# Kernel tuning notes

Hardware: AMD Instinct MI355X
Metric: run time of the kernel (lower is better)

Reference implementation:

```python
import jax, jax.numpy as jnp
import numpy as np

HEAD = 4

def setup_inputs() -> dict:
    key = jax.random.key(0)
    ks = jax.random.split(key, 6)
    b, h, w, dim, attn_dim = 2, 64, 64, 256, 128
    return {
        "query": jax.random.normal(ks[0], (b, h, w, dim), jnp.float32),
        "context": jax.random.normal(ks[1], (b, h, w, dim), jnp.float32),
        "Wq": jax.random.normal(ks[2], (dim, attn_dim), jnp.float32) * (dim ** -0.5),
        "Wk": jax.random.normal(ks[3], (dim, attn_dim), jnp.float32) * (dim ** -0.5),
        "Wv": jax.random.normal(ks[4], (dim, attn_dim), jnp.float32) * (dim ** -0.5),
        "Wo": jax.random.normal(ks[5], (attn_dim, dim), jnp.float32) * (attn_dim ** -0.5),
    }

def reference(query, context, Wq, Wk, Wv, Wo):
    b, h, w, c = query.shape
    attn_dim = Wq.shape[1]
    head = HEAD
    head_dim = attn_dim // head
    scale = head_dim ** -0.5
    n = h * w
    # 1x1 conv, no bias == per-pixel dense projection
    q = (query.reshape(b, n, c) @ Wq).reshape(b, n, head, head_dim)
    k = (context.reshape(b, n, c) @ Wk).reshape(b, n, head, head_dim)
    v = (context.reshape(b, n, c) @ Wv).reshape(b, n, head, head_dim)
    score = jnp.einsum('bihd,bjhd->bijh', q, k) * scale  # [b, n, n, head]
    attn = jax.nn.softmax(score, axis=-2)  # softmax over key axis j
    out = jnp.einsum('bijh,bjhd->bihd', attn, v).reshape(b, n, attn_dim)
    return (out @ Wo).reshape(b, h, w, c)
```

## Files before the change

kernel.cpp:

```cpp
#include <hip/hip_runtime.h>
#include <hip/hip_bf16.h>
#include <math.h>

#define N_TOK 4096
#define C_DIM 256
#define A_DIM 128
#define HEADS 4
#define HD    32
#define NBAT  2
#define BH    (NBAT * HEADS)

#define SCALE_LOG2E 0.25503521f

#define SPLITS 8
#define KEYS_PER_SPLIT (N_TOK / SPLITS)

#define KS 40
#define VS 72
#define PS 40

typedef __attribute__((ext_vector_type(8))) short short8;
typedef __attribute__((ext_vector_type(4))) short short4_t;
typedef __attribute__((ext_vector_type(4))) float floatx4;

__device__ __forceinline__ unsigned short f2bf(float f) {
    unsigned int u = __float_as_uint(f);
    u = (u + 0x7fffu + ((u >> 16) & 1u)) >> 16;
    return (unsigned short)u;
}
__device__ __forceinline__ float bf2f(unsigned short u) {
    return __uint_as_float((unsigned int)u << 16);
}
__device__ __forceinline__ unsigned int pack2(float a, float b) {
    unsigned int lo = (__float_as_uint(a) + 0x8000u) >> 16;
    unsigned int hi = (__float_as_uint(b) + 0x8000u) & 0xffff0000u;
    return hi | lo;
}

__global__ __launch_bounds__(256) void wpack_kernel(
    const float* __restrict__ Wq, const float* __restrict__ Wk,
    const float* __restrict__ Wv, const float* __restrict__ Wo,
    unsigned short* __restrict__ Wp)
{
    const int chunk = blockIdx.x * 256 + threadIdx.x;
    const int wid = chunk >> 12;
    const int c = chunk & 4095;
    const int lane = c & 63, quad = lane >> 4, l15 = lane & 15;
    short8 v;
    if (wid < 3) {
        const int s = c >> 9, t = (c >> 6) & 7;
        const float* W = (wid == 0) ? Wq : ((wid == 1) ? Wk : Wv);
        const float scale = (wid == 0) ? SCALE_LOG2E : 1.0f;
        const int src = (s * 32 + quad * 8) * A_DIM + t * 16 + l15;
        #pragma unroll
        for (int j = 0; j < 8; j++) v[j] = (short)f2bf(W[src + j * A_DIM] * scale);
    } else {
        const int s = c >> 10, t = (c >> 6) & 15;
        const int src = (s * 32 + quad * 8) * C_DIM + t * 16 + l15;
        #pragma unroll
        for (int j = 0; j < 8; j++) v[j] = (short)f2bf(Wo[src + j * C_DIM]);
    }
    *(short8*)(Wp + (long)chunk * 8) = v;
}

__global__ __launch_bounds__(256) void qkv_kernel(
    const float* __restrict__ query, const float* __restrict__ context,
    const unsigned short* __restrict__ Wp,
    unsigned short* __restrict__ Qb, unsigned short* __restrict__ Kb,
    unsigned short* __restrict__ Vb)
{
    __shared__ __align__(16) unsigned short V_lds[128 * 18];

    const int tid = threadIdx.x;
    const int w = tid >> 6, lane = tid & 63;
    const int quad = lane >> 4, l15 = lane & 15;
    const int ch = w;
    const long i0 = (long)blockIdx.x * 16;
    const long row = i0 + l15;

    const unsigned short* Wqp = Wp;
    const unsigned short* Wkp = Wp + 32768;
    const unsigned short* Wvp = Wp + 65536;

    floatx4 aQ[2] = {}, aK[2] = {}, aV[2] = {};

    for (int s = 0; s < 8; s++) {
        const float* qp = query + row * C_DIM + s * 32 + quad * 8;
        const float* cp = context + row * C_DIM + s * 32 + quad * 8;
        floatx4 q0 = *(const floatx4*)qp, q1 = *(const floatx4*)(qp + 4);
        floatx4 c0 = *(const floatx4*)cp, c1 = *(const floatx4*)(cp + 4);
        short8 aq, ac;
        #pragma unroll
        for (int j = 0; j < 4; j++) {
            aq[j] = (short)f2bf(q0[j]); aq[4 + j] = (short)f2bf(q1[j]);
            ac[j] = (short)f2bf(c0[j]); ac[4 + j] = (short)f2bf(c1[j]);
        }
        #pragma unroll
        for (int tp = 0; tp < 2; tp++) {
            const long fo = ((long)(s * 8 + ch * 2 + tp) * 64 + lane) * 8;
            short8 bq = *(const short8*)(Wqp + fo);
            short8 bk = *(const short8*)(Wkp + fo);
            short8 bv = *(const short8*)(Wvp + fo);
            aQ[tp] = __builtin_amdgcn_mfma_f32_16x16x32_bf16(aq, bq, aQ[tp], 0, 0, 0);
            aK[tp] = __builtin_amdgcn_mfma_f32_16x16x32_bf16(ac, bk, aK[tp], 0, 0, 0);
            aV[tp] = __builtin_amdgcn_mfma_f32_16x16x32_bf16(ac, bv, aV[tp], 0, 0, 0);
        }
    }

    const long b = i0 >> 12;
    const long n0 = i0 & (N_TOK - 1);
    const long nbase = n0 + quad * 4;
    #pragma unroll
    for (int tp = 0; tp < 2; tp++) {
        const int col = ch * 32 + tp * 16 + l15;
        const int h = col >> 5, d = col & 31;
        unsigned short* qdst = Qb + ((b * HEADS + h) * N_TOK + nbase) * HD + d;
        unsigned short* kdst = Kb + ((b * HEADS + h) * N_TOK + nbase) * HD + d;
        #pragma unroll
        for (int r = 0; r < 4; r++) {
            qdst[r * HD] = f2bf(aQ[tp][r]);
            kdst[r * HD] = f2bf(aK[tp][r]);
        }
        short4_t pv;
        #pragma unroll
        for (int r = 0; r < 4; r++) pv[r] = (short)f2bf(aV[tp][r]);
        *(short4_t*)&V_lds[col * 18 + quad * 4] = pv;
    }
    __syncthreads();

    {
        const int col = tid >> 1, seg = tid & 1;
        const int h = col >> 5, d = col & 31;
        unsigned short* dst = Vb + ((b * HEADS + h) * HD + d) * N_TOK + n0 + seg * 8;
        *(short8*)dst = *(const short8*)&V_lds[col * 18 + seg * 8];
    }
}

__global__ __launch_bounds__(256, 4) void attn_kernel(
    const unsigned short* __restrict__ Qb, const unsigned short* __restrict__ Kb,
    const unsigned short* __restrict__ Vb,
    unsigned short* __restrict__ AO, float* __restrict__ Lbuf)
{
    __shared__ __align__(16) unsigned short K_lds[64 * KS];
    __shared__ __align__(16) unsigned short V_lds[HD * VS];
    __shared__ __align__(16) unsigned short P_lds[4][2][2 * 16 * PS];

    const int tid  = threadIdx.x;
    const int w    = tid >> 6;
    const int lane = tid & 63;
    const int quad = lane >> 4;
    const int l15  = lane & 15;

    const int L  = blockIdx.x;
    const int g  = (L & 7) + 8 * ((L >> 3) >> 5);
    const int qb = (L >> 3) & 31;
    const int bh = g & 7;
    const int z  = g >> 3;
    const int i0 = qb * 128 + w * 32;

    const unsigned short* Qh = Qb + (long)bh * N_TOK * HD;
    const unsigned short* Kh = Kb + (long)bh * N_TOK * HD;
    const unsigned short* Vh = Vb + (long)bh * HD * N_TOK;

    const short8 qfA = *(const short8*)(Qh + (long)(i0 + l15) * HD + quad * 8);
    const short8 qfB = *(const short8*)(Qh + (long)(i0 + 16 + l15) * HD + quad * 8);

    floatx4 accA0 = {0.f,0.f,0.f,0.f}, accA1 = {0.f,0.f,0.f,0.f};
    floatx4 accB0 = {0.f,0.f,0.f,0.f}, accB1 = {0.f,0.f,0.f,0.f};
    float lAc = 0.f, lBc = 0.f;

    const int  kst = (tid >> 2) * KS + (tid & 3) * 8;
    const int  vst = (tid >> 3) * VS + (tid & 7) * 8;
    const long vgl = (long)(tid >> 3) * N_TOK + (tid & 7) * 8;
    const int  pwb = l15 * (PS / 2);

    const int j_lo = z * KEYS_PER_SPLIT, j_hi = j_lo + KEYS_PER_SPLIT;

    short8 kreg = *(const short8*)(Kh + (long)j_lo * HD + tid * 8);
    short8 vreg = *(const short8*)(Vh + vgl + j_lo);

    for (int j0 = j_lo; j0 < j_hi; j0 += 64) {
        __syncthreads();
        *(short8*)&K_lds[kst] = kreg;
        *(short8*)&V_lds[vst] = vreg;
        if (j0 + 64 < j_hi) {
            kreg = *(const short8*)(Kh + (long)(j0 + 64) * HD + tid * 8);
            vreg = *(const short8*)(Vh + vgl + j0 + 64);
        }
        __syncthreads();

        #pragma unroll
        for (int sub = 0; sub < 2; sub++) {
            const int jb = sub * 32;
            short8 kf0 = *(short8*)&K_lds[(jb + l15) * KS + quad * 8];
            short8 kf1 = *(short8*)&K_lds[(jb + 16 + l15) * KS + quad * 8];
            const floatx4 zf = {0.f,0.f,0.f,0.f};
            floatx4 sA0 = __builtin_amdgcn_mfma_f32_16x16x32_bf16(kf0, qfA, zf, 0, 0, 0);
            floatx4 sA1 = __builtin_amdgcn_mfma_f32_16x16x32_bf16(kf1, qfA, zf, 0, 0, 0);
            floatx4 sB0 = __builtin_amdgcn_mfma_f32_16x16x32_bf16(kf0, qfB, zf, 0, 0, 0);
            floatx4 sB1 = __builtin_amdgcn_mfma_f32_16x16x32_bf16(kf1, qfB, zf, 0, 0, 0);

            floatx4 pA0, pA1, pB0, pB1;
            #pragma unroll
            for (int r = 0; r < 4; r++) {
                pA0[r] = __builtin_amdgcn_exp2f(sA0[r]);
                pA1[r] = __builtin_amdgcn_exp2f(sA1[r]);
                pB0[r] = __builtin_amdgcn_exp2f(sB0[r]);
                pB1[r] = __builtin_amdgcn_exp2f(sB1[r]);
                lAc += pA0[r] + pA1[r];
                lBc += pB0[r] + pB1[r];
            }

            unsigned int* Pq = (unsigned int*)&P_lds[w][sub][0];
            Pq[pwb + quad * 2 + 0]       = pack2(pA0[0], pA0[1]);
            Pq[pwb + quad * 2 + 1]       = pack2(pA0[2], pA0[3]);
            Pq[pwb + 8 + quad * 2 + 0]   = pack2(pA1[0], pA1[1]);
            Pq[pwb + 8 + quad * 2 + 1]   = pack2(pA1[2], pA1[3]);
            Pq[320 + pwb + quad * 2 + 0] = pack2(pB0[0], pB0[1]);
            Pq[320 + pwb + quad * 2 + 1] = pack2(pB0[2], pB0[3]);
            Pq[320 + pwb + 8 + quad * 2 + 0] = pack2(pB1[0], pB1[1]);
            Pq[320 + pwb + 8 + quad * 2 + 1] = pack2(pB1[2], pB1[3]);

            short8 pfA = *(short8*)&P_lds[w][sub][l15 * PS + quad * 8];
            short8 pfB = *(short8*)&P_lds[w][sub][16 * PS + l15 * PS + quad * 8];

            short8 vf0 = *(short8*)&V_lds[l15 * VS + jb + quad * 8];
            short8 vf1 = *(short8*)&V_lds[(16 + l15) * VS + jb + quad * 8];
            accA0 = __builtin_amdgcn_mfma_f32_16x16x32_bf16(pfA, vf0, accA0, 0, 0, 0);
            accA1 = __builtin_amdgcn_mfma_f32_16x16x32_bf16(pfA, vf1, accA1, 0, 0, 0);
            accB0 = __builtin_amdgcn_mfma_f32_16x16x32_bf16(pfB, vf0, accB0, 0, 0, 0);
            accB1 = __builtin_amdgcn_mfma_f32_16x16x32_bf16(pfB, vf1, accB1, 0, 0, 0);
        }
    }

    lAc += __shfl_xor(lAc, 16); lAc += __shfl_xor(lAc, 32);
    lBc += __shfl_xor(lBc, 16); lBc += __shfl_xor(lBc, 32);

    const int b = bh >> 2, h = bh & 3;
    unsigned short* AOz = AO + (long)z * (NBAT * N_TOK * A_DIM);
    float* Lz = Lbuf + (long)z * (BH * N_TOK);
    if (quad == 0) {
        Lz[(long)bh * N_TOK + i0 + l15]      = lAc;
        Lz[(long)bh * N_TOK + i0 + 16 + l15] = lBc;
    }
    #pragma unroll
    for (int r = 0; r < 4; r++) {
        const float invA = 1.0f / __shfl(lAc, quad * 4 + r);
        const float invB = 1.0f / __shfl(lBc, quad * 4 + r);
        const long rowA = (long)b * N_TOK + i0 + quad * 4 + r;
        const long rowB = rowA + 16;
        AOz[rowA * A_DIM + h * HD + l15]      = f2bf(accA0[r] * invA);
        AOz[rowA * A_DIM + h * HD + 16 + l15] = f2bf(accA1[r] * invA);
        AOz[rowB * A_DIM + h * HD + l15]      = f2bf(accB0[r] * invB);
        AOz[rowB * A_DIM + h * HD + 16 + l15] = f2bf(accB1[r] * invB);
    }
}

__global__ __launch_bounds__(256) void outproj_kernel(
    const unsigned short* __restrict__ AO, const float* __restrict__ Lbuf,
    const unsigned short* __restrict__ Wp, float* __restrict__ out)
{
    const int tid = threadIdx.x;
    const int w = tid >> 6, lane = tid & 63;
    const int quad = lane >> 4, l15 = lane & 15;
    const int ch = w;
    const long i0 = (long)blockIdx.x * 16;
    const long row = i0 + l15;
    const int b = (int)(row >> 12);
    const int n = (int)(row & (N_TOK - 1));
    const unsigned short* Wop = Wp + 98304;

    floatx4 acc[4] = {};

    #pragma unroll
    for (int s = 0; s < 4; s++) {
        float lz[SPLITS], lsum = 0.f;
        #pragma unroll
        for (int z = 0; z < SPLITS; z++) {
            lz[z] = Lbuf[(long)z * (BH * N_TOK) + (long)(b * HEADS + s) * N_TOK + n];
            lsum += lz[z];
        }
        const float inv = 1.0f / lsum;
        float vals[8] = {};
        #pragma unroll
        for (int z = 0; z < SPLITS; z++) {
            short8 az = *(const short8*)(AO + (long)z * (NBAT * N_TOK * A_DIM) +
                                         row * A_DIM + s * 32 + quad * 8);
            const float wz = lz[z] * inv;
            #pragma unroll
            for (int j = 0; j < 8; j++) vals[j] += wz * bf2f((unsigned short)az[j]);
        }
        short8 af;
        #pragma unroll
        for (int j = 0; j < 8; j++) af[j] = (short)f2bf(vals[j]);
        #pragma unroll
        for (int tp = 0; tp < 4; tp++) {
            const int t = ch * 4 + tp;
            short8 bo = *(const short8*)(Wop + ((long)(s * 16 + t) * 64 + lane) * 8);
            acc[tp] = __builtin_amdgcn_mfma_f32_16x16x32_bf16(af, bo, acc[tp], 0, 0, 0);
        }
    }

    #pragma unroll
    for (int tp = 0; tp < 4; tp++) {
        #pragma unroll
        for (int r = 0; r < 4; r++)
            out[(i0 + quad * 4 + r) * C_DIM + (ch * 4 + tp) * 16 + l15] = acc[tp][r];
    }
}

extern "C" void kernel_launch(void* const* d_in, const int* in_sizes, int n_in,
                              void* d_out, int out_size, void* d_ws, size_t ws_size,
                              hipStream_t stream)
{
    const float* query   = (const float*)d_in[0];
    const float* context = (const float*)d_in[1];
    const float* Wq      = (const float*)d_in[2];
    const float* Wk      = (const float*)d_in[3];
    const float* Wv      = (const float*)d_in[4];
    const float* Wo      = (const float*)d_in[5];
    float* out = (float*)d_out;

    char* ws = (char*)d_ws;
    unsigned short* Qb = (unsigned short*)(ws);
    unsigned short* Kb = (unsigned short*)(ws + (2 << 20));
    unsigned short* Vb = (unsigned short*)(ws + (4 << 20));
    unsigned short* AO = (unsigned short*)(ws + (6 << 20));
    float*          Lb = (float*)(ws + (22 << 20));
    unsigned short* Wp = (unsigned short*)(ws + (23 << 20));

    wpack_kernel<<<dim3(64), dim3(256), 0, stream>>>(Wq, Wk, Wv, Wo, Wp);
    qkv_kernel<<<dim3(512), dim3(256), 0, stream>>>(query, context, Wp, Qb, Kb, Vb);
    attn_kernel<<<dim3(32 * BH * SPLITS), dim3(256), 0, stream>>>(
        Qb, Kb, Vb, AO, Lb);
    outproj_kernel<<<dim3(512), dim3(256), 0, stream>>>(AO, Lb, Wp, out);
}
```

Measured before the change: 126.6 us.

## Drop LDS staging in attention: load K/V fragments directly, transpose P via permlane

Removes shared-memory staging of K and V tiles and the per-tile barriers. Each wave now loads its MFMA operand fragments straight from global memory. The P matrix round-trip through LDS is replaced by an in-register cross-lane transpose using permlane swaps, with a shuffle/swizzle fallback. This cuts LDS traffic and synchronisation but makes each wave issue redundant global loads of K/V (4 waves per block read the same keys) with no software prefetch, relying on L1/L2 caching.

```diff
diff --git a/kernel.cpp b/kernel.cpp
--- a/kernel.cpp
+++ b/kernel.cpp
@@ -15,10 +15,6 @@
 #define SPLITS 8
 #define KEYS_PER_SPLIT (N_TOK / SPLITS)
 
-#define KS 40
-#define VS 72
-#define PS 40
-
 typedef __attribute__((ext_vector_type(8))) short short8;
 typedef __attribute__((ext_vector_type(4))) short short4_t;
 typedef __attribute__((ext_vector_type(4))) float floatx4;
@@ -35,6 +31,39 @@
     unsigned int lo = (__float_as_uint(a) + 0x8000u) >> 16;
     unsigned int hi = (__float_as_uint(b) + 0x8000u) & 0xffff0000u;
     return hi | lo;
+}
+
+__device__ __forceinline__ short8 quad_xpose(unsigned int a0, unsigned int a1,
+                                             unsigned int a2, unsigned int a3,
+                                             int lane)
+{
+    union { unsigned int u[4]; short8 s; } cv;
+#if __has_builtin(__builtin_amdgcn_permlane32_swap) && __has_builtin(__builtin_amdgcn_permlane16_swap)
+    (void)lane;
+    auto s0 = __builtin_amdgcn_permlane32_swap(a0, a2, false, false);
+    auto s1 = __builtin_amdgcn_permlane32_swap(a1, a3, false, false);
+    auto t0 = __builtin_amdgcn_permlane16_swap(s0[0], s0[1], false, false);
+    auto t1 = __builtin_amdgcn_permlane16_swap(s1[0], s1[1], false, false);
+    cv.u[0] = t0[0]; cv.u[1] = t1[0]; cv.u[2] = t0[1]; cv.u[3] = t1[1];
+#else
+    const int hi32 = (lane >> 5) & 1;
+    const int u16  = (lane >> 4) & 1;
+    unsigned int x0 = __shfl_xor(a2, 32), x2 = __shfl_xor(a0, 32);
+    unsigned int r0 = hi32 ? x0 : a0;
+    unsigned int r1 = hi32 ? a2 : x2;
+    unsigned int y0 = __shfl_xor(a3, 32), y2 = __shfl_xor(a1, 32);
+    unsigned int r0b = hi32 ? y0 : a1;
+    unsigned int r1b = hi32 ? a3 : y2;
+    unsigned int w0 = (unsigned int)__builtin_amdgcn_ds_swizzle((int)r1, 0x401F);
+    unsigned int w1 = (unsigned int)__builtin_amdgcn_ds_swizzle((int)r0, 0x401F);
+    unsigned int w2 = (unsigned int)__builtin_amdgcn_ds_swizzle((int)r1b, 0x401F);
+    unsigned int w3 = (unsigned int)__builtin_amdgcn_ds_swizzle((int)r0b, 0x401F);
+    cv.u[0] = u16 ? w0 : r0;
+    cv.u[1] = u16 ? w2 : r0b;
+    cv.u[2] = u16 ? r1 : w1;
+    cv.u[3] = u16 ? r1b : w3;
+#endif
+    return cv.s;
 }
 
 __global__ __launch_bounds__(256) void wpack_kernel(
@@ -141,10 +170,6 @@
     const unsigned short* __restrict__ Vb,
     unsigned short* __restrict__ AO, float* __restrict__ Lbuf)
 {
-    __shared__ __align__(16) unsigned short K_lds[64 * KS];
-    __shared__ __align__(16) unsigned short V_lds[HD * VS];
-    __shared__ __align__(16) unsigned short P_lds[4][2][2 * 16 * PS];
-
     const int tid  = threadIdx.x;
     const int w    = tid >> 6;
     const int lane = tid & 63;
@@ -169,31 +194,31 @@
     floatx4 accB0 = {0.f,0.f,0.f,0.f}, accB1 = {0.f,0.f,0.f,0.f};
     float lAc = 0.f, lBc = 0.f;
 
-    const int  kst = (tid >> 2) * KS + (tid & 3) * 8;
-    const int  vst = (tid >> 3) * VS + (tid & 7) * 8;
-    const long vgl = (long)(tid >> 3) * N_TOK + (tid & 7) * 8;
-    const int  pwb = l15 * (PS / 2);
-
-    const int j_lo = z * KEYS_PER_SPLIT, j_hi = j_lo + KEYS_PER_SPLIT;
-
-    short8 kreg = *(const short8*)(Kh + (long)j_lo * HD + tid * 8);
-    short8 vreg = *(const short8*)(Vh + vgl + j_lo);
-
-    for (int j0 = j_lo; j0 < j_hi; j0 += 64) {
-        __syncthreads();
-        *(short8*)&K_lds[kst] = kreg;
-        *(short8*)&V_lds[vst] = vreg;
-        if (j0 + 64 < j_hi) {
-            kreg = *(const short8*)(Kh + (long)(j0 + 64) * HD + tid * 8);
-            vreg = *(const short8*)(Vh + vgl + j0 + 64);
-        }
-        __syncthreads();
+    const int j_lo = z * KEYS_PER_SPLIT;
+
+    const unsigned short* kp  = Kh + (long)j_lo * HD + l15 * HD + quad * 8;
+    const unsigned short* vp0 = Vh + (long)l15 * N_TOK + j_lo + quad * 8;
+    const unsigned short* vp1 = vp0 + 16 * N_TOK;
+
+    #pragma unroll 1
+    for (int t = 0; t < KEYS_PER_SPLIT / 64; ++t) {
+        const short8 k00 = *(const short8*)(kp);
+        const short8 k10 = *(const short8*)(kp + 16 * HD);
+        const short8 k01 = *(const short8*)(kp + 32 * HD);
+        const short8 k11 = *(const short8*)(kp + 48 * HD);
+        const short8 v00 = *(const short8*)(vp0);
+        const short8 v10 = *(const short8*)(vp1);
+        const short8 v01 = *(const short8*)(vp0 + 32);
+        const short8 v11 = *(const short8*)(vp1 + 32);
+        kp += 64 * HD; vp0 += 64; vp1 += 64;
 
         #pragma unroll
         for (int sub = 0; sub < 2; sub++) {
-            const int jb = sub * 32;
-            short8 kf0 = *(short8*)&K_lds[(jb + l15) * KS + quad * 8];
-            short8 kf1 = *(short8*)&K_lds[(jb + 16 + l15) * KS + quad * 8];
+            const short8 kf0 = sub ? k01 : k00;
+            const short8 kf1 = sub ? k11 : k10;
+            const short8 vf0 = sub ? v01 : v00;
+            const short8 vf1 = sub ? v11 : v10;
+
             const floatx4 zf = {0.f,0.f,0.f,0.f};
             floatx4 sA0 = __builtin_amdgcn_mfma_f32_16x16x32_bf16(kf0, qfA, zf, 0, 0, 0);
             floatx4 sA1 = __builtin_amdgcn_mfma_f32_16x16x32_bf16(kf1, qfA, zf, 0, 0, 0);
@@ -211,21 +236,11 @@
                 lBc += pB0[r] + pB1[r];
             }
 
-            unsigned int* Pq = (unsigned int*)&P_lds[w][sub][0];
-            Pq[pwb + quad * 2 + 0]       = pack2(pA0[0], pA0[1]);
-            Pq[pwb + quad * 2 + 1]       = pack2(pA0[2], pA0[3]);
-            Pq[pwb + 8 + quad * 2 + 0]   = pack2(pA1[0], pA1[1]);
-            Pq[pwb + 8 + quad * 2 + 1]   = pack2(pA1[2], pA1[3]);
-            Pq[320 + pwb + quad * 2 + 0] = pack2(pB0[0], pB0[1]);
-            Pq[320 + pwb + quad * 2 + 1] = pack2(pB0[2], pB0[3]);
-            Pq[320 + pwb + 8 + quad * 2 + 0] = pack2(pB1[0], pB1[1]);
-            Pq[320 + pwb + 8 + quad * 2 + 1] = pack2(pB1[2], pB1[3]);
-
-            short8 pfA = *(short8*)&P_lds[w][sub][l15 * PS + quad * 8];
-            short8 pfB = *(short8*)&P_lds[w][sub][16 * PS + l15 * PS + quad * 8];
-
-            short8 vf0 = *(short8*)&V_lds[l15 * VS + jb + quad * 8];
-            short8 vf1 = *(short8*)&V_lds[(16 + l15) * VS + jb + quad * 8];
+            short8 pfA = quad_xpose(pack2(pA0[0], pA0[1]), pack2(pA0[2], pA0[3]),
+                                    pack2(pA1[0], pA1[1]), pack2(pA1[2], pA1[3]), lane);
+            short8 pfB = quad_xpose(pack2(pB0[0], pB0[1]), pack2(pB0[2], pB0[3]),
+                                    pack2(pB1[0], pB1[1]), pack2(pB1[2], pB1[3]), lane);
+
             accA0 = __builtin_amdgcn_mfma_f32_16x16x32_bf16(pfA, vf0, accA0, 0, 0, 0);
             accA1 = __builtin_amdgcn_mfma_f32_16x16x32_bf16(pfA, vf1, accA1, 0, 0, 0);
             accB0 = __builtin_amdgcn_mfma_f32_16x16x32_bf16(pfB, vf0, accB0, 0, 0, 0);
```

After: 148.0 us. 1.17x slower.
